# Optimization experiments

Measured on AMD Instinct MI355X. Metric: run time of the kernel, lower is better.

The kernel has to match this reference:

```python
import jax, jax.numpy as jnp
import numpy as np

B, S, HID = 2, 2048, 1024
NH, NKV = 16, 4
HD = HID // NH          # 64
NREP = NH // NKV        # 4
EPS = 1e-06


def _rotate_half(x):
    h = x.shape[-1] // 2
    return jnp.concatenate([-x[..., h:], x[..., :h]], axis=-1)


def _rope(q, k, cos, sin):
    # q: [b,s,h,d], k: [b,s,kv,d]; cos/sin: [s,d] -> unsqueeze head dim
    c = cos[:, None, :]
    s = sin[:, None, :]
    return q * c + _rotate_half(q) * s, k * c + _rotate_half(k) * s


def setup_inputs() -> dict:
    key = jax.random.key(0)
    ks = jax.random.split(key, 8)
    sc = 0.02
    return {
        "x": jax.random.normal(ks[0], (B, S, HID), jnp.float32),
        "cos": jnp.cos(jnp.arange(S, dtype=jnp.float32)[:, None] *
                       (1.0 / (1e6 ** (jnp.arange(HD, dtype=jnp.float32) / HD)))),
        "sin": jnp.sin(jnp.arange(S, dtype=jnp.float32)[:, None] *
                       (1.0 / (1e6 ** (jnp.arange(HD, dtype=jnp.float32) / HD)))),
        "attention_mask": jnp.ones((B, S), jnp.int32),
        "Wq": jax.random.normal(ks[1], (HID, NH * HD), jnp.float32) * sc,
        "Wk": jax.random.normal(ks[2], (HID, NKV * HD), jnp.float32) * sc,
        "Wv": jax.random.normal(ks[3], (HID, NKV * HD), jnp.float32) * sc,
        "Wo": jax.random.normal(ks[4], (NH * HD, HID), jnp.float32) * sc,
    }


def reference(x, cos, sin, attention_mask, Wq, Wk, Wv, Wo):
    b, s, _ = x.shape
    q = (x @ Wq).reshape(b, s, NH, HD)
    k = (x @ Wk).reshape(b, s, NKV, HD)
    v = (x @ Wv).reshape(b, s, NKV, HD)
    q, k = _rope(q, k, cos[:s], sin[:s])
    # GQA repeat: [b,s,kv,d] -> [b,s,h,d]
    k = jnp.repeat(k, NREP, axis=2)
    v = jnp.repeat(v, NREP, axis=2)
    # -> [b,h,s,d]
    q = jnp.transpose(q, (0, 2, 1, 3))
    k = jnp.transpose(k, (0, 2, 1, 3))
    v = jnp.transpose(v, (0, 2, 1, 3))
    # feature map: elu(x) + 1 (positive features)
    q = jax.nn.elu(q) + 1.0
    k = jax.nn.elu(k) + 1.0
    # prefill path (seq_len > 1): non-causal kernelized scores
    scores = jnp.einsum("bhsd,bhtd->bhst", q, k)  # [b,h,s,s]
    mask = attention_mask[:, None, None, :]       # [b,1,1,s]
    scores = jnp.where(mask == 0, 0.0, scores)
    denom = jnp.clip(
        jax.lax.stop_gradient(jnp.abs(scores).sum(-1, keepdims=True)), 1e-06, None)
    scores = scores / denom
    out = jnp.einsum("bhst,bhtd->bhsd", scores, v)
    out = jnp.transpose(out, (0, 2, 1, 3)).reshape(b, s, NH * HD)
    return out @ Wo
```

## Files before the change

kernel.cpp:

```cpp
#include <hip/hip_runtime.h>
#include <hip/hip_bf16.h>

using u16 = unsigned short;
using u32 = unsigned int;

namespace {
constexpr int S   = 2048;
constexpr int HID = 1024;
constexpr int M   = 4096;
constexpr int K   = 1024;
}

typedef __attribute__((ext_vector_type(8))) short short8;
typedef __attribute__((ext_vector_type(4))) float f32x4;

__device__ __forceinline__ u16 f2bf(float f) {
    u32 u = __builtin_bit_cast(u32, f);
    u += 0x7fffu + ((u >> 16) & 1u);
    return (u16)(u >> 16);
}
__device__ __forceinline__ float bf2f(u16 h) {
    return __builtin_bit_cast(float, (u32)h << 16);
}
__device__ __forceinline__ float phi(float x) {
    return x > 0.f ? x + 1.f : __expf(x);
}
__device__ __forceinline__ void glds16(const u16* g, u16* l) {
    __builtin_amdgcn_global_load_lds(
        (const __attribute__((address_space(1))) u32*)g,
        (__attribute__((address_space(3))) u32*)l, 16, 0, 0);
}

template <int MODE>
__global__ __launch_bounds__(256, 3) void gemm_k(
    const u16* __restrict__ A, const u16* __restrict__ B,
    u16* __restrict__ Cq, float* __restrict__ Ckv,
    float* __restrict__ Cf, int ldc, int zAr, int zBr, int zCr,
    const float* __restrict__ Cos, const float* __restrict__ Sin,
    const int* __restrict__ Mask)
{
    constexpr int BK = 64;
    constexpr int NT = K / BK;
    __shared__ __align__(16) u16 sA0[64 * BK],  sA1[64 * BK];
    __shared__ __align__(16) u16 sB0[128 * BK], sB1[128 * BK];

    A += (size_t)blockIdx.z * zAr * K;
    B += (size_t)blockIdx.z * zBr * K;
    if (MODE == 1) Cf += (size_t)blockIdx.z * zCr * ldc;

    const int tid  = threadIdx.x;
    const int lane = tid & 63, w = tid >> 6;
    const int wm = w & 1, wn = w >> 1;
    const int m0 = blockIdx.x * 64, n0 = blockIdx.y * 128;
    const int fr = lane & 15, fq = lane >> 4;

    const int srow  = lane >> 3;
    const int sslot = lane & 7;
    const int sswz  = (sslot ^ srow) * 8;

    const u16* Asrc = A + (size_t)(m0 + w * 8 + srow) * K + sswz;
    const u16* Bsrc = B + (size_t)(n0 + w * 8 + srow) * K + sswz;
    const int ldsb = (w * 8) * BK;

    f32x4 acc[2][4] = {};

#define STAGE(dA, dB, kt)                                          \
    do {                                                           \
        glds16(Asrc + (kt),                 dA + ldsb);            \
        glds16(Asrc + (size_t)32 * K + (kt), dA + 32 * BK + ldsb); \
        glds16(Bsrc + (kt),                 dB + ldsb);            \
        glds16(Bsrc + (size_t)32 * K + (kt), dB + 32 * BK + ldsb); \
        glds16(Bsrc + (size_t)64 * K + (kt), dB + 64 * BK + ldsb); \
        glds16(Bsrc + (size_t)96 * K + (kt), dB + 96 * BK + ldsb); \
    } while (0)

#define COMPUTE(sAc, sBc)                                                    \
    do {                                                                     \
        _Pragma("unroll")                                                    \
        for (int kk = 0; kk < 2; ++kk) {                                     \
            const int ks = ((kk * 4 + fq) ^ (fr & 7)) * 8;                   \
            short8 ah[2], bh[4];                                             \
            _Pragma("unroll")                                                \
            for (int i = 0; i < 2; ++i)                                      \
                ah[i] = *(const short8*)(sAc + (wm * 32 + i * 16 + fr) * BK + ks); \
            _Pragma("unroll")                                                \
            for (int j = 0; j < 4; ++j)                                      \
                bh[j] = *(const short8*)(sBc + (wn * 64 + j * 16 + fr) * BK + ks); \
            _Pragma("unroll")                                                \
            for (int i = 0; i < 2; ++i)                                      \
                _Pragma("unroll")                                            \
                for (int j = 0; j < 4; ++j)                                  \
                    acc[i][j] = __builtin_amdgcn_mfma_f32_16x16x32_bf16(     \
                        ah[i], bh[j], acc[i][j], 0, 0, 0);                   \
        }                                                                    \
    } while (0)

#define SYNC()                                              \
    do {                                                    \
        asm volatile("s_waitcnt vmcnt(0)" ::: "memory");    \
        __syncthreads();                                    \
    } while (0)

    STAGE(sA0, sB0, 0);
    SYNC();
#pragma unroll 1
    for (int t = 0; t < NT; t += 2) {
        if (t + 1 < NT) STAGE(sA1, sB1, (t + 1) * BK);
        COMPUTE(sA0, sB0);
        SYNC();
        if (t + 2 < NT) STAGE(sA0, sB0, (t + 2) * BK);
        COMPUTE(sA1, sB1);
        SYNC();
    }
#undef STAGE
#undef COMPUTE
#undef SYNC

    const bool isQ = (MODE == 0) && (n0 < 1024);
    const bool isK = (MODE == 0) && (n0 >= 1024) && (n0 < 1280);
#pragma unroll
    for (int i = 0; i < 2; ++i)
#pragma unroll
        for (int jj = 0; jj < 4; ++jj) {
            const int row = m0 + wm * 32 + i * 16 + fq * 4 + jj;
            float v0 = acc[i][0][jj], v1 = acc[i][1][jj];
            float v2 = acc[i][2][jj], v3 = acc[i][3][jj];
            if (MODE == 1) {
                float* cr = &Cf[(size_t)row * ldc + n0 + wn * 64 + fr];
                cr[0] = v0; cr[16] = v1; cr[32] = v2; cr[48] = v3;
                continue;
            }
            if (isQ || isK) {
                const int sb = (row & (S - 1)) * 64;
                float r0 = v0 * Cos[sb + fr]      - v2 * Sin[sb + fr];
                float r2 = v2 * Cos[sb + fr + 32] + v0 * Sin[sb + fr + 32];
                float r1 = v1 * Cos[sb + fr + 16] - v3 * Sin[sb + fr + 16];
                float r3 = v3 * Cos[sb + fr + 48] + v1 * Sin[sb + fr + 48];
                v0 = phi(r0); v1 = phi(r1); v2 = phi(r2); v3 = phi(r3);
            }
            if (isQ) {
                u16* cr = &Cq[(size_t)row * 1024 + n0 + wn * 64 + fr];
                cr[0]  = f2bf(v0); cr[16] = f2bf(v1);
                cr[32] = f2bf(v2); cr[48] = f2bf(v3);
            } else if (isK) {
                const float mv = (float)Mask[row];
                float* cr = &Ckv[(size_t)row * 512 + (n0 - 1024) + wn * 64 + fr];
                cr[0] = v0 * mv; cr[16] = v1 * mv;
                cr[32] = v2 * mv; cr[48] = v3 * mv;
            } else {
                float* cr = &Ckv[(size_t)row * 512 + 256 + (n0 - 1280) + wn * 64 + fr];
                cr[0] = v0; cr[16] = v1; cr[32] = v2; cr[48] = v3;
            }
        }
}

__global__ __launch_bounds__(256) void prep_k(
    const float* __restrict__ X,  u16* __restrict__ Xb,
    const float* __restrict__ Wq, const float* __restrict__ Wk,
    const float* __restrict__ Wv, const float* __restrict__ Wo,
    u16* __restrict__ wt, u16* __restrict__ wot)
{
    const int bid = blockIdx.x, tid = threadIdx.x;
    if (bid < 4096) {
        const int i = (bid * 256 + tid) * 4;
        float4 v = *reinterpret_cast<const float4*>(&X[i]);
        ushort4 h;
        h.x = f2bf(v.x); h.y = f2bf(v.y); h.z = f2bf(v.z); h.w = f2bf(v.w);
        *reinterpret_cast<ushort4*>(&Xb[i]) = h;
        return;
    }
    int r = bid - 4096;
    const float* W; u16* T; int N, nbase, bx, by;
    if (r < 1024)      { W = Wq; T = wt;  N = 1024; nbase = 0;    bx = r & 31; by = r >> 5; }
    else if (r < 1280) { r -= 1024; W = Wk; T = wt; N = 256; nbase = 1024; bx = r & 7; by = r >> 3; }
    else if (r < 1536) { r -= 1280; W = Wv; T = wt; N = 256; nbase = 1280; bx = r & 7; by = r >> 3; }
    else               { r -= 1536; W = Wo; T = wot; N = 1024; nbase = 0;  bx = r & 31; by = r >> 5; }

    __shared__ float t[32][33];
    const int n0 = bx * 32, k0 = by * 32;
    const int tx = tid & 31, ty = tid >> 5;
#pragma unroll
    for (int i = 0; i < 4; ++i)
        t[ty + i * 8][tx] = W[(size_t)(k0 + ty + i * 8) * N + n0 + tx];
    __syncthreads();
#pragma unroll
    for (int i = 0; i < 4; ++i) {
        const int n = ty + i * 8;
        T[(size_t)(nbase + n0 + n) * 1024 + k0 + tx] = f2bf(t[tx][n]);
    }
}

__global__ __launch_bounds__(256) void kv_stage1_k(
    const float* __restrict__ KVf, float* __restrict__ part)
{
    const int g  = blockIdx.x;
    const int ch = blockIdx.y;
    const int b  = g >> 2, kvh = g & 3;
    const int tid = threadIdx.x;

    __shared__ float ks[64][64];
    __shared__ float vs[64][64];
    const int m0 = b * S + ch * 64;
#pragma unroll
    for (int l = 0; l < 4; ++l) {
        int idx = tid + l * 256;
        int r = idx >> 4, q4 = (idx & 15) * 4;
        const float* src = KVf + (size_t)(m0 + r) * 512 + kvh * 64;
        *reinterpret_cast<float4*>(&ks[r][q4]) = *reinterpret_cast<const float4*>(src + q4);
        *reinterpret_cast<float4*>(&vs[r][q4]) = *reinterpret_cast<const float4*>(src + 256 + q4);
    }
    __syncthreads();

    const int i = tid >> 2, j0 = (tid & 3) * 16;
    float4 a0 = {0,0,0,0}, a1 = {0,0,0,0}, a2 = {0,0,0,0}, a3 = {0,0,0,0};
#pragma unroll 8
    for (int r = 0; r < 64; ++r) {
        float kv = ks[r][i];
        float4 w0 = *reinterpret_cast<const float4*>(&vs[r][j0]);
        float4 w1 = *reinterpret_cast<const float4*>(&vs[r][j0 + 4]);
        float4 w2 = *reinterpret_cast<const float4*>(&vs[r][j0 + 8]);
        float4 w3 = *reinterpret_cast<const float4*>(&vs[r][j0 + 12]);
        a0.x = fmaf(kv, w0.x, a0.x); a0.y = fmaf(kv, w0.y, a0.y);
        a0.z = fmaf(kv, w0.z, a0.z); a0.w = fmaf(kv, w0.w, a0.w);
        a1.x = fmaf(kv, w1.x, a1.x); a1.y = fmaf(kv, w1.y, a1.y);
        a1.z = fmaf(kv, w1.z, a1.z); a1.w = fmaf(kv, w1.w, a1.w);
        a2.x = fmaf(kv, w2.x, a2.x); a2.y = fmaf(kv, w2.y, a2.y);
        a2.z = fmaf(kv, w2.z, a2.z); a2.w = fmaf(kv, w2.w, a2.w);
        a3.x = fmaf(kv, w3.x, a3.x); a3.y = fmaf(kv, w3.y, a3.y);
        a3.z = fmaf(kv, w3.z, a3.z); a3.w = fmaf(kv, w3.w, a3.w);
    }
    float* dst = part + ((size_t)g * 32 + ch) * 4160;
    float* d0 = dst + i * 64 + j0;
    *reinterpret_cast<float4*>(d0)      = a0;
    *reinterpret_cast<float4*>(d0 + 4)  = a1;
    *reinterpret_cast<float4*>(d0 + 8)  = a2;
    *reinterpret_cast<float4*>(d0 + 12) = a3;
    if (tid < 64) {
        float ksum = 0.f;
#pragma unroll 8
        for (int r = 0; r < 64; ++r) ksum += ks[r][tid];
        dst[4096 + tid] = ksum;
    }
}

__global__ __launch_bounds__(256) void kv_reduce_k(
    const float* __restrict__ part, u16* __restrict__ KVh,
    float* __restrict__ Ksumf)
{
    const int g = blockIdx.x;
    const int e = blockIdx.y * 256 + threadIdx.x;
    if (e >= 4160) return;
    const float* p = part + (size_t)g * 32 * 4160 + e;
    float s = 0.f;
#pragma unroll 8
    for (int c = 0; c < 32; ++c) s += p[(size_t)c * 4160];
    if (e < 4096) KVh[g * 4096 + e] = f2bf(s);
    else          Ksumf[g * 64 + (e - 4096)] = s;
}

__global__ __launch_bounds__(256, 2) void kw_gemm_k(
    const u16* __restrict__ WoT, const u16* __restrict__ KVb,
    u16* __restrict__ KWT)
{
    __shared__ __align__(16) u16 sA[128 * 64];
    __shared__ __align__(16) u16 sB[64 * 64];

    const int tid = threadIdx.x, lane = tid & 63, w = tid >> 6;
    const int o0 = blockIdx.x * 128;
    const int gh = blockIdx.y, b = gh >> 4, h = gh & 15, g = b * 4 + (h >> 2);
    const int fr = lane & 15, fq = lane >> 4;
    const int srow = lane >> 3, sslot = lane & 7;
    const int sswz = (sslot ^ srow) * 8;

#pragma unroll
    for (int c = 0; c < 4; ++c) {
        const int rb = w * 32 + c * 8;
        glds16(WoT + (size_t)(o0 + rb + srow) * 1024 + h * 64 + sswz, sA + rb * 64);
    }
#pragma unroll
    for (int c = 0; c < 2; ++c) {
        const int rb = w * 16 + c * 8;
        glds16(KVb + (size_t)g * 4096 + (rb + srow) * 64 + sswz, sB + rb * 64);
    }
    asm volatile("s_waitcnt vmcnt(0)" ::: "memory");
    __syncthreads();

    f32x4 acc[2][4] = {};
#pragma unroll
    for (int kk = 0; kk < 2; ++kk) {
        short8 a_h[2], b_h[4];
#pragma unroll
        for (int i = 0; i < 2; ++i) {
            const int row = w * 32 + i * 16 + fr;
            a_h[i] = *(const short8*)(sA + row * 64 + ((kk * 4 + fq) ^ (fr & 7)) * 8);
        }
#pragma unroll
        for (int j = 0; j < 4; ++j) {
            const int row = j * 16 + fr;
            b_h[j] = *(const short8*)(sB + row * 64 + ((kk * 4 + fq) ^ (fr & 7)) * 8);
        }
#pragma unroll
        for (int i = 0; i < 2; ++i)
#pragma unroll
            for (int j = 0; j < 4; ++j)
                acc[i][j] = __builtin_amdgcn_mfma_f32_16x16x32_bf16(
                    a_h[i], b_h[j], acc[i][j], 0, 0, 0);
    }
#pragma unroll
    for (int i = 0; i < 2; ++i)
#pragma unroll
        for (int j = 0; j < 4; ++j)
#pragma unroll
            for (int jj = 0; jj < 4; ++jj) {
                const int row = o0 + w * 32 + i * 16 + fq * 4 + jj;
                const int col = j * 16 + fr;
                KWT[((size_t)b * 1024 + row) * 1024 + h * 64 + col] =
                    f2bf(acc[i][j][jj]);
            }
}

__global__ __launch_bounds__(256) void qhat_k(
    const u16* __restrict__ Qt, const float* __restrict__ Ksumf,
    u16* __restrict__ Qh)
{
    const int t = blockIdx.x * 256 + threadIdx.x;
    const int m = t >> 4, h = t & 15;
    const int g = (m >> 11) * 4 + (h >> 2);
    const u16* q  = Qt + (size_t)m * 1024 + h * 64;
    const float* Ks = Ksumf + g * 64;

    float qv[64];
    float den = 0.f;
#pragma unroll
    for (int c = 0; c < 8; ++c) {
        short8 v8 = *reinterpret_cast<const short8*>(q + c * 8);
#pragma unroll
        for (int j = 0; j < 8; ++j) {
            qv[c * 8 + j] = bf2f((u16)v8[j]);
            den = fmaf(qv[c * 8 + j], Ks[c * 8 + j], den);
        }
    }
    const float rd = 1.f / fmaxf(den, 1e-6f);
    u16* o = Qh + (size_t)m * 1024 + h * 64;
#pragma unroll
    for (int c = 0; c < 8; ++c) {
        short8 ov;
#pragma unroll
        for (int j = 0; j < 8; ++j) ov[j] = (short)f2bf(qv[c * 8 + j] * rd);
        *reinterpret_cast<short8*>(o + c * 8) = ov;
    }
}

extern "C" void kernel_launch(void* const* d_in, const int* in_sizes, int n_in,
                              void* d_out, int out_size, void* d_ws, size_t ws_size,
                              hipStream_t stream)
{
    const float* x    = (const float*)d_in[0];
    const float* cosp = (const float*)d_in[1];
    const float* sinp = (const float*)d_in[2];
    const int*   msk  = (const int*)d_in[3];
    const float* Wq   = (const float*)d_in[4];
    const float* Wk   = (const float*)d_in[5];
    const float* Wv   = (const float*)d_in[6];
    const float* Wo   = (const float*)d_in[7];
    float* out = (float*)d_out;

    u16* xbf  = (u16*)d_ws;
    u16* wt   = xbf  + (size_t)M * K;
    u16* wot  = wt   + (size_t)1536 * K;
    u16* qt   = wot  + (size_t)K * K;
    u16* qhat = qt   + (size_t)M * K;
    u16* kvb  = qhat + (size_t)M * K;
    u16* kwt  = kvb  + 8 * 4096;
    float* kvf   = (float*)(kwt + (size_t)2 * K * K);
    float* part  = kvf + (size_t)M * 512;
    float* ksumf = part + (size_t)8 * 32 * 4160;

    prep_k<<<4096 + 1024 + 256 + 256 + 1024, 256, 0, stream>>>(
        x, xbf, Wq, Wk, Wv, Wo, wt, wot);

    gemm_k<0><<<dim3(M / 64, 1536 / 128, 1), 256, 0, stream>>>(
        xbf, wt, qt, kvf, nullptr, 0, 0, 0, 0, cosp, sinp, msk);

    kv_stage1_k<<<dim3(8, 32), 256, 0, stream>>>(kvf, part);
    kv_reduce_k<<<dim3(8, 17), 256, 0, stream>>>(part, kvb, ksumf);

    kw_gemm_k<<<dim3(8, 32), 256, 0, stream>>>(wot, kvb, kwt);

    qhat_k<<<(M * 16) / 256, 256, 0, stream>>>(qt, ksumf, qhat);

    gemm_k<1><<<dim3(2048 / 64, HID / 128, 2), 256, 0, stream>>>(
        qhat, kwt, nullptr, nullptr, out, HID, 2048, 1024, 2048,
        nullptr, nullptr, nullptr);
}
```

Before: 70.14 us.

## Use 32x32 MFMA in GEMMs, remap workgroups across XCDs, fuse kw-gemm with qhat

The main GEMM kernel moves from 16x16x32 to 32x32x16 bf16 MFMA tiles with two accumulators per wave, which cuts LDS fragment reads per MFMA, and the epilogue is rewritten for the new accumulator layout. Workgroup IDs are remapped round-robin over 8 chunks so that neighbouring tiles land on the same XCD and share L2. The kw_gemm and qhat kernels are merged into one launch with block-range dispatch, saving a kernel launch and letting the two independent pieces run concurrently. The risks are higher register pressure from f32x16 accumulators under launch_bounds(256,3), and the swizzle assumes the workgroup count is divisible by 8.

New measurement: 73.26 us. 1.04x slower.

```diff
diff --git a/kernel.cpp b/kernel.cpp
--- a/kernel.cpp
+++ b/kernel.cpp
@@ -11,8 +11,9 @@
 constexpr int K   = 1024;
 }
 
-typedef __attribute__((ext_vector_type(8))) short short8;
-typedef __attribute__((ext_vector_type(4))) float f32x4;
+typedef __attribute__((ext_vector_type(8)))  short short8;
+typedef __attribute__((ext_vector_type(4)))  float f32x4;
+typedef __attribute__((ext_vector_type(16))) float f32x16;
 
 __device__ __forceinline__ u16 f2bf(float f) {
     u32 u = __builtin_bit_cast(u32, f);
@@ -44,15 +45,23 @@
     __shared__ __align__(16) u16 sA0[64 * BK],  sA1[64 * BK];
     __shared__ __align__(16) u16 sB0[128 * BK], sB1[128 * BK];
 
-    A += (size_t)blockIdx.z * zAr * K;
-    B += (size_t)blockIdx.z * zBr * K;
-    if (MODE == 1) Cf += (size_t)blockIdx.z * zCr * ldc;
+    const int gx = gridDim.x, gy = gridDim.y;
+    const int nwg  = gx * gy * gridDim.z;
+    const int orig = blockIdx.x + gx * (blockIdx.y + gy * blockIdx.z);
+    const int wgid = (orig & 7) * (nwg >> 3) + (orig >> 3);
+    const int bx = wgid % gx;
+    const int rest = wgid / gx;
+    const int by = rest % gy, bz = rest / gy;
+
+    A += (size_t)bz * zAr * K;
+    B += (size_t)bz * zBr * K;
+    if (MODE == 1) Cf += (size_t)bz * zCr * ldc;
 
     const int tid  = threadIdx.x;
     const int lane = tid & 63, w = tid >> 6;
     const int wm = w & 1, wn = w >> 1;
-    const int m0 = blockIdx.x * 64, n0 = blockIdx.y * 128;
-    const int fr = lane & 15, fq = lane >> 4;
+    const int m0 = bx * 64, n0 = by * 128;
+    const int l31 = lane & 31, khalf = lane >> 5, l7 = lane & 7;
 
     const int srow  = lane >> 3;
     const int sslot = lane & 7;
@@ -62,7 +71,9 @@
     const u16* Bsrc = B + (size_t)(n0 + w * 8 + srow) * K + sswz;
     const int ldsb = (w * 8) * BK;
 
-    f32x4 acc[2][4] = {};
+    f32x16 acc0 = {}, acc1 = {};
+    const int arow = wm * 32 + l31;
+    const int brow0 = wn * 64 + l31, brow1 = brow0 + 32;
 
 #define STAGE(dA, dB, kt)                                          \
     do {                                                           \
@@ -77,21 +88,14 @@
 #define COMPUTE(sAc, sBc)                                                    \
     do {                                                                     \
         _Pragma("unroll")                                                    \
-        for (int kk = 0; kk < 2; ++kk) {                                     \
-            const int ks = ((kk * 4 + fq) ^ (fr & 7)) * 8;                   \
-            short8 ah[2], bh[4];                                             \
-            _Pragma("unroll")                                                \
-            for (int i = 0; i < 2; ++i)                                      \
-                ah[i] = *(const short8*)(sAc + (wm * 32 + i * 16 + fr) * BK + ks); \
-            _Pragma("unroll")                                                \
-            for (int j = 0; j < 4; ++j)                                      \
-                bh[j] = *(const short8*)(sBc + (wn * 64 + j * 16 + fr) * BK + ks); \
-            _Pragma("unroll")                                                \
-            for (int i = 0; i < 2; ++i)                                      \
-                _Pragma("unroll")                                            \
-                for (int j = 0; j < 4; ++j)                                  \
-                    acc[i][j] = __builtin_amdgcn_mfma_f32_16x16x32_bf16(     \
-                        ah[i], bh[j], acc[i][j], 0, 0, 0);                   \
+        for (int st = 0; st < 4; ++st) {                                     \
+            const int slot = st * 2 + khalf;              \
+            const int ks = (slot ^ l7) * 8;           \
+            short8 a  = *(const short8*)(sAc + arow  * BK + ks);             \
+            short8 b0 = *(const short8*)(sBc + brow0 * BK + ks);             \
+            short8 b1 = *(const short8*)(sBc + brow1 * BK + ks);             \
+            acc0 = __builtin_amdgcn_mfma_f32_32x32x16_bf16(a, b0, acc0, 0, 0, 0); \
+            acc1 = __builtin_amdgcn_mfma_f32_32x32x16_bf16(a, b1, acc1, 0, 0, 0); \
         }                                                                    \
     } while (0)
 
@@ -118,40 +122,34 @@
 
     const bool isQ = (MODE == 0) && (n0 < 1024);
     const bool isK = (MODE == 0) && (n0 >= 1024) && (n0 < 1280);
-#pragma unroll
-    for (int i = 0; i < 2; ++i)
-#pragma unroll
-        for (int jj = 0; jj < 4; ++jj) {
-            const int row = m0 + wm * 32 + i * 16 + fq * 4 + jj;
-            float v0 = acc[i][0][jj], v1 = acc[i][1][jj];
-            float v2 = acc[i][2][jj], v3 = acc[i][3][jj];
-            if (MODE == 1) {
-                float* cr = &Cf[(size_t)row * ldc + n0 + wn * 64 + fr];
-                cr[0] = v0; cr[16] = v1; cr[32] = v2; cr[48] = v3;
-                continue;
-            }
-            if (isQ || isK) {
-                const int sb = (row & (S - 1)) * 64;
-                float r0 = v0 * Cos[sb + fr]      - v2 * Sin[sb + fr];
-                float r2 = v2 * Cos[sb + fr + 32] + v0 * Sin[sb + fr + 32];
-                float r1 = v1 * Cos[sb + fr + 16] - v3 * Sin[sb + fr + 16];
-                float r3 = v3 * Cos[sb + fr + 48] + v1 * Sin[sb + fr + 48];
-                v0 = phi(r0); v1 = phi(r1); v2 = phi(r2); v3 = phi(r3);
-            }
-            if (isQ) {
-                u16* cr = &Cq[(size_t)row * 1024 + n0 + wn * 64 + fr];
-                cr[0]  = f2bf(v0); cr[16] = f2bf(v1);
-                cr[32] = f2bf(v2); cr[48] = f2bf(v3);
-            } else if (isK) {
-                const float mv = (float)Mask[row];
-                float* cr = &Ckv[(size_t)row * 512 + (n0 - 1024) + wn * 64 + fr];
-                cr[0] = v0 * mv; cr[16] = v1 * mv;
-                cr[32] = v2 * mv; cr[48] = v3 * mv;
-            } else {
-                float* cr = &Ckv[(size_t)row * 512 + 256 + (n0 - 1280) + wn * 64 + fr];
-                cr[0] = v0; cr[16] = v1; cr[32] = v2; cr[48] = v3;
-            }
-        }
+    const int colb = n0 + wn * 64 + l31;
+#pragma unroll
+    for (int r = 0; r < 16; ++r) {
+        const int row = m0 + wm * 32 + (r & 3) + 8 * (r >> 2) + 4 * khalf;
+        float v0 = acc0[r], v1 = acc1[r];
+        if (MODE == 1) {
+            float* cr = &Cf[(size_t)row * ldc + colb];
+            cr[0] = v0; cr[32] = v1;
+            continue;
+        }
+        if (isQ || isK) {
+            const int sb = (row & (S - 1)) * 64;
+            float r0 = v0 * Cos[sb + l31]      - v1 * Sin[sb + l31];
+            float r1 = v1 * Cos[sb + l31 + 32] + v0 * Sin[sb + l31 + 32];
+            v0 = phi(r0); v1 = phi(r1);
+        }
+        if (isQ) {
+            u16* cr = &Cq[(size_t)row * 1024 + colb];
+            cr[0] = f2bf(v0); cr[32] = f2bf(v1);
+        } else if (isK) {
+            const float mv = (float)Mask[row];
+            float* cr = &Ckv[(size_t)row * 512 + (colb - 1024)];
+            cr[0] = v0 * mv; cr[32] = v1 * mv;
+        } else {
+            float* cr = &Ckv[(size_t)row * 512 + 256 + (colb - 1280)];
+            cr[0] = v0; cr[32] = v1;
+        }
+    }
 }
 
 __global__ __launch_bounds__(256) void prep_k(
@@ -258,16 +256,48 @@
     else          Ksumf[g * 64 + (e - 4096)] = s;
 }
 
-__global__ __launch_bounds__(256, 2) void kw_gemm_k(
+__global__ __launch_bounds__(256) void kwqhat_k(
     const u16* __restrict__ WoT, const u16* __restrict__ KVb,
-    u16* __restrict__ KWT)
-{
+    u16* __restrict__ KWT,
+    const u16* __restrict__ Qt, const float* __restrict__ Ksumf,
+    u16* __restrict__ Qh)
+{
+    const int tid = threadIdx.x;
+    if (blockIdx.x >= 256) {
+        const int t = (blockIdx.x - 256) * 256 + tid;
+        const int m = t >> 4, h = t & 15;
+        const int g = (m >> 11) * 4 + (h >> 2);
+        const u16* q  = Qt + (size_t)m * 1024 + h * 64;
+        const float* Ks = Ksumf + g * 64;
+
+        float qv[64];
+        float den = 0.f;
+#pragma unroll
+        for (int c = 0; c < 8; ++c) {
+            short8 v8 = *reinterpret_cast<const short8*>(q + c * 8);
+#pragma unroll
+            for (int j = 0; j < 8; ++j) {
+                qv[c * 8 + j] = bf2f((u16)v8[j]);
+                den = fmaf(qv[c * 8 + j], Ks[c * 8 + j], den);
+            }
+        }
+        const float rd = 1.f / fmaxf(den, 1e-6f);
+        u16* o = Qh + (size_t)m * 1024 + h * 64;
+#pragma unroll
+        for (int c = 0; c < 8; ++c) {
+            short8 ov;
+#pragma unroll
+            for (int j = 0; j < 8; ++j) ov[j] = (short)f2bf(qv[c * 8 + j] * rd);
+            *reinterpret_cast<short8*>(o + c * 8) = ov;
+        }
+        return;
+    }
     __shared__ __align__(16) u16 sA[128 * 64];
     __shared__ __align__(16) u16 sB[64 * 64];
 
-    const int tid = threadIdx.x, lane = tid & 63, w = tid >> 6;
-    const int o0 = blockIdx.x * 128;
-    const int gh = blockIdx.y, b = gh >> 4, h = gh & 15, g = b * 4 + (h >> 2);
+    const int lane = tid & 63, w = tid >> 6;
+    const int o0 = (blockIdx.x & 7) * 128;
+    const int gh = blockIdx.x >> 3, b = gh >> 4, h = gh & 15, g = b * 4 + (h >> 2);
     const int fr = lane & 15, fq = lane >> 4;
     const int srow = lane >> 3, sslot = lane & 7;
     const int sswz = (sslot ^ srow) * 8;
@@ -317,38 +347,6 @@
                 KWT[((size_t)b * 1024 + row) * 1024 + h * 64 + col] =
                     f2bf(acc[i][j][jj]);
             }
-}
-
-__global__ __launch_bounds__(256) void qhat_k(
-    const u16* __restrict__ Qt, const float* __restrict__ Ksumf,
-    u16* __restrict__ Qh)
-{
-    const int t = blockIdx.x * 256 + threadIdx.x;
-    const int m = t >> 4, h = t & 15;
-    const int g = (m >> 11) * 4 + (h >> 2);
-    const u16* q  = Qt + (size_t)m * 1024 + h * 64;
-    const float* Ks = Ksumf + g * 64;
-
-    float qv[64];
-    float den = 0.f;
-#pragma unroll
-    for (int c = 0; c < 8; ++c) {
-        short8 v8 = *reinterpret_cast<const short8*>(q + c * 8);
-#pragma unroll
-        for (int j = 0; j < 8; ++j) {
-            qv[c * 8 + j] = bf2f((u16)v8[j]);
-            den = fmaf(qv[c * 8 + j], Ks[c * 8 + j], den);
-        }
-    }
-    const float rd = 1.f / fmaxf(den, 1e-6f);
-    u16* o = Qh + (size_t)m * 1024 + h * 64;
-#pragma unroll
-    for (int c = 0; c < 8; ++c) {
-        short8 ov;
-#pragma unroll
-        for (int j = 0; j < 8; ++j) ov[j] = (short)f2bf(qv[c * 8 + j] * rd);
-        *reinterpret_cast<short8*>(o + c * 8) = ov;
-    }
 }
 
 extern "C" void kernel_launch(void* const* d_in, const int* in_sizes, int n_in,
@@ -385,9 +383,7 @@
     kv_stage1_k<<<dim3(8, 32), 256, 0, stream>>>(kvf, part);
     kv_reduce_k<<<dim3(8, 17), 256, 0, stream>>>(part, kvb, ksumf);
 
-    kw_gemm_k<<<dim3(8, 32), 256, 0, stream>>>(wot, kvb, kwt);
-
-    qhat_k<<<(M * 16) / 256, 256, 0, stream>>>(qt, ksumf, qhat);
+    kwqhat_k<<<512, 256, 0, stream>>>(wot, kvb, kwt, qt, ksumf, qhat);
 
     gemm_k<1><<<dim3(2048 / 64, HID / 128, 2), 256, 0, stream>>>(
         qhat, kwt, nullptr, nullptr, out, HID, 2048, 1024, 2048,
```
